# Optimization experiments

Hardware: AMD Instinct MI355X
Metric: run time of the kernel (lower is better)

Reference implementation:

```python
import jax, jax.numpy as jnp
import numpy as np


def setup_inputs() -> dict:
    key = jax.random.key(0)
    k1, k2 = jax.random.split(key)
    B, S_ENC, S_DEC, D = 8, 2048, 2048, 1024
    enc_outputs = jax.random.normal(k1, (B, S_ENC, D), dtype=jnp.float32)
    dec_outputs = jax.random.normal(k2, (B, S_DEC, D), dtype=jnp.float32)
    return {"enc_outputs": enc_outputs, "dec_outputs": dec_outputs}


def reference(enc_outputs, dec_outputs):
    # scores: [B, S_enc, S_dec] = enc @ dec^T (unscaled)
    a_t = jnp.einsum('bed,btd->bet', enc_outputs, dec_outputs)
    a_t = jax.nn.softmax(a_t, axis=-1)
    # context: [B, S_dec, D] = a_t^T @ enc
    c_t = jnp.einsum('bet,bed->btd', a_t, enc_outputs)
    return c_t
```

## Files before the change

### kernel.cpp

```cpp
#include <hip/hip_runtime.h>


typedef _Float16 half8 __attribute__((ext_vector_type(8)));
typedef _Float16 half4v __attribute__((ext_vector_type(4)));
typedef float floatx4 __attribute__((ext_vector_type(4)));

__device__ __forceinline__ void async_load16(const _Float16* g, void* l) {
  __builtin_amdgcn_global_load_lds(
      (const __attribute__((address_space(1))) void*)g,
      (__attribute__((address_space(3))) void*)l, 16, 0, 0);
}

template <typename OutT, bool NORM, bool STATS>
__global__ __launch_bounds__(512, 2) void gemm8p(
    const _Float16* __restrict__ A, const _Float16* __restrict__ Bt,
    OutT* __restrict__ C, const float* __restrict__ cstat,
    float2* __restrict__ part_out, int K, long strideA, long strideB,
    long strideC, int ldA, int ldB, int ldC) {
  extern __shared__ char smem_[];
  const int tid = threadIdx.x;
  const int lane = tid & 63;
  const int wave = tid >> 6;
  const int wm = wave >> 2;
  const int wn = wave & 3;
  const int l15 = lane & 15;
  const int lh = lane >> 4;

  const int gx = gridDim.x, gxy = gridDim.x * gridDim.y;
  int fid = blockIdx.z * gxy + blockIdx.y * gx + blockIdx.x;
  const int nwg = gxy * gridDim.z;
  fid = (fid & 7) * (nwg >> 3) + (fid >> 3);
  const int b = fid / gxy;
  const int rem = fid - b * gxy;
  const int m0 = (rem / gx) * 256;
  const int n0 = (rem % gx) * 256;

  A += (long)b * strideA + (long)m0 * ldA;
  Bt += (long)b * strideB + (long)n0 * ldB;
  C += (long)b * strideC;
  const float* cstatB = NORM ? cstat + (size_t)b * 2048 : nullptr;

  const int lb0 = l15 * 128 + ((lh ^ (l15 & 7)) << 4);
  const int lb1 = lb0 ^ 64;
  const char* aBuf[2] = {smem_ + wm * 16384, smem_ + 32768 + wm * 16384};
  const char* bBuf[2] = {
      smem_ + 65536 + (wn >> 1) * 16384 + (wn & 1) * 8192,
      smem_ + 98304 + (wn >> 1) * 16384 + (wn & 1) * 8192};
  char* aSlot[2] = {smem_, smem_ + 32768};
  char* bSlot[2] = {smem_ + 65536, smem_ + 98304};
  char* cLds = smem_ + 131072;

  const int srow = tid >> 3;
  const int skk = ((tid & 7) ^ (srow & 7)) << 3;
  const _Float16* Ast = A + (long)srow * ldA + skk;
  const _Float16* Bst = Bt + (long)srow * ldB + skk;
  const int dst = tid << 4;

  floatx4 acc[8][4] = {};
  half8 a[4][2], b0[2][2], b1[2][2];

  auto stage = [&](const _Float16* gs, int ld, int k0, char* slot) {
#pragma unroll
    for (int i = 0; i < 4; ++i)
      async_load16(gs + (long)(i * 64) * ld + k0, slot + i * 8192 + dst);
  };
  auto mm = [&](int mh, int nh, half8(&bb)[2][2]) {
    __builtin_amdgcn_s_setprio(1);
#pragma unroll
    for (int s = 0; s < 2; ++s)
#pragma unroll
      for (int q = 0; q < 4; ++q)
#pragma unroll
        for (int n = 0; n < 2; ++n)
          acc[mh * 4 + q][nh * 2 + n] = __builtin_amdgcn_mfma_f32_16x16x32_f16(
              a[q][s], bb[n][s], acc[mh * 4 + q][nh * 2 + n], 0, 0, 0);
    __builtin_amdgcn_s_setprio(0);
  };
  auto bar = [&]() { asm volatile("s_barrier" ::: "memory"); };

  auto quad4 = [&](int cur, int kst, int ebase, bool last) {
    const char* aB_ = aBuf[cur];
    const char* bB_ = bBuf[cur];
    if constexpr (NORM) {
      const int co = (ebase + skk) << 2;
      const float4 c0 = *(const float4*)(cLds + co);
      const float4 c1 = *(const float4*)(cLds + co + 16);
      const float cc[8] = {c0.x, c0.y, c0.z, c0.w, c1.x, c1.y, c1.z, c1.w};
#pragma unroll
      for (int i = 0; i < 4; ++i) {
        char* p = aSlot[cur] + i * 8192 + dst;
        half8 v = *(const half8*)p;
        half8 o;
#pragma unroll
        for (int j = 0; j < 8; ++j)
          o[j] = (_Float16)exp2f((float)v[j] * 1.44269504f + cc[j]);
        *(half8*)p = o;
      }
      asm volatile("s_waitcnt lgkmcnt(0)" ::: "memory");
      bar();
    }
#pragma unroll
    for (int q = 0; q < 4; ++q) {
      a[q][0] = *(const half8*)(aB_ + lb0 + q * 2048);
      a[q][1] = *(const half8*)(aB_ + lb1 + q * 2048);
    }
#pragma unroll
    for (int n = 0; n < 2; ++n) {
      b0[n][0] = *(const half8*)(bB_ + lb0 + n * 2048);
      b0[n][1] = *(const half8*)(bB_ + lb1 + n * 2048);
      b1[n][0] = *(const half8*)(bB_ + lb0 + (n + 2) * 2048);
      b1[n][1] = *(const half8*)(bB_ + lb1 + (n + 2) * 2048);
    }
    bar();
    mm(0, 0, b0);
    bar();
    bar();
    mm(0, 1, b1);
    bar();
#pragma unroll
    for (int q = 0; q < 4; ++q) {
      a[q][0] = *(const half8*)(aB_ + lb0 + (q + 4) * 2048);
      a[q][1] = *(const half8*)(aB_ + lb1 + (q + 4) * 2048);
    }
    if (kst >= 0) stage(Bst, ldB, kst, bSlot[cur]);
    bar();
    mm(1, 1, b1);
    bar();
    if (kst >= 0) stage(Ast, ldA, kst, aSlot[cur]);
    mm(1, 0, b0);
    if (last)
      asm volatile("s_waitcnt vmcnt(0)" ::: "memory");
    else
      asm volatile("s_waitcnt vmcnt(8)" ::: "memory");
    bar();
  };

  float4 cv;
  if constexpr (NORM) cv = *(const float4*)(cstatB + tid * 4);
  stage(Ast, ldA, 0, aSlot[0]);
  stage(Bst, ldB, 0, bSlot[0]);
  stage(Ast, ldA, 64, aSlot[1]);
  stage(Bst, ldB, 64, bSlot[1]);
  if constexpr (NORM) *(float4*)(cLds + (tid << 4)) = cv;
  asm volatile("s_waitcnt vmcnt(8) lgkmcnt(0)" ::: "memory");
  bar();

  const int NT = K >> 6;
  for (int i = 0; i < (NT >> 1) - 1; ++i) {
    quad4(0, (2 * i + 2) * 64, (2 * i) * 64, false);
    quad4(1, (2 * i + 3) * 64, (2 * i + 1) * 64, false);
  }
  quad4(0, -1, (NT - 2) * 64, true);
  quad4(1, -1, (NT - 1) * 64, true);

#pragma unroll
  for (int mf = 0; mf < 8; ++mf) {
    const long r0 = (long)(m0 + wm * 128 + mf * 16 + lh * 4);
#pragma unroll
    for (int nf = 0; nf < 4; ++nf) {
      const int cc = n0 + wn * 64 + nf * 16 + l15;
#pragma unroll
      for (int rr = 0; rr < 4; ++rr)
        C[(r0 + rr) * ldC + cc] = (OutT)acc[mf][nf][rr];
    }
  }

  if constexpr (STATS) {
    float2* sm = (float2*)smem_;
#pragma unroll
    for (int nf = 0; nf < 4; ++nf) {
      float x16[8][4];
#pragma unroll
      for (int mf = 0; mf < 8; ++mf)
#pragma unroll
        for (int rr = 0; rr < 4; ++rr)
          x16[mf][rr] = (float)(_Float16)acc[mf][nf][rr];
      float mx = -1e30f;
#pragma unroll
      for (int mf = 0; mf < 8; ++mf)
#pragma unroll
        for (int rr = 0; rr < 4; ++rr) mx = fmaxf(mx, x16[mf][rr]);
      float ss = 0.f;
#pragma unroll
      for (int mf = 0; mf < 8; ++mf)
#pragma unroll
        for (int rr = 0; rr < 4; ++rr) ss += __expf(x16[mf][rr] - mx);
#pragma unroll
      for (int d = 16; d <= 32; d <<= 1) {
        const float om = __shfl_xor(mx, d, 64);
        const float os = __shfl_xor(ss, d, 64);
        const float m2 = fmaxf(mx, om);
        ss = ss * __expf(mx - m2) + os * __expf(om - m2);
        mx = m2;
      }
      if (lh == 0) sm[wm * 256 + wn * 64 + nf * 16 + l15] = make_float2(mx, ss);
    }
    __syncthreads();
    if (tid < 256) {
      const float2 a0 = sm[tid], a1 = sm[256 + tid];
      const float m2 = fmaxf(a0.x, a1.x);
      const float s2 =
          a0.y * __expf(a0.x - m2) + a1.y * __expf(a1.x - m2);
      part_out[(size_t)(m0 >> 8) * 16384 + (size_t)b * 2048 + n0 + tid] =
          make_float2(m2, s2);
    }
  }
}

__global__ __launch_bounds__(256) void conv_enc(const float* __restrict__ E,
                                                _Float16* __restrict__ Eh,
                                                _Float16* __restrict__ EhT,
                                                int Se, int D) {
  __shared__ _Float16 T[64][72];
  const int b = blockIdx.z;
  const int d0 = blockIdx.x * 64;
  const int e0 = blockIdx.y * 64;
  const float* Eb = E + (size_t)b * Se * D;
  _Float16* Ehb = Eh + (size_t)b * Se * D;
  _Float16* EhTb = EhT + (size_t)b * D * Se;
  const int tid = threadIdx.x;
  const int tx = tid & 15;
  const int ty = tid >> 4;

  half4v h[4];
#pragma unroll
  for (int r = 0; r < 4; ++r) {
    const int e = e0 + ty * 4 + r;
    float4 v = *(const float4*)(Eb + (size_t)e * D + d0 + tx * 4);
    h[r][0] = (_Float16)v.x; h[r][1] = (_Float16)v.y;
    h[r][2] = (_Float16)v.z; h[r][3] = (_Float16)v.w;
    *(half4v*)(Ehb + (size_t)e * D + d0 + tx * 4) = h[r];
  }
#pragma unroll
  for (int c = 0; c < 4; ++c) {
    half4v w;
#pragma unroll
    for (int r = 0; r < 4; ++r) w[r] = h[r][c];
    *(half4v*)&T[tx * 4 + c][ty * 4] = w;
  }
  __syncthreads();
#pragma unroll
  for (int p = 0; p < 2; ++p) {
    const int idx = tid + p * 256;
    const int row = idx >> 3;
    const int ck = idx & 7;
    *(half8*)(EhTb + (size_t)(d0 + row) * Se + e0 + ck * 8) =
        *(const half8*)&T[row][ck * 8];
  }
}

__global__ __launch_bounds__(256) void conv_dec(const float* __restrict__ X,
                                                _Float16* __restrict__ Y) {
  const size_t i = ((size_t)blockIdx.x * 256 + threadIdx.x) * 8;
  float4 a = *(const float4*)(X + i);
  float4 b = *(const float4*)(X + i + 4);
  half8 h;
  h[0] = (_Float16)a.x; h[1] = (_Float16)a.y;
  h[2] = (_Float16)a.z; h[3] = (_Float16)a.w;
  h[4] = (_Float16)b.x; h[5] = (_Float16)b.y;
  h[6] = (_Float16)b.z; h[7] = (_Float16)b.w;
  *(half8*)(Y + i) = h;
}

__global__ __launch_bounds__(256) void stats_combine(
    const float2* __restrict__ part, float* __restrict__ cstat) {
  const int idx = blockIdx.x * 256 + threadIdx.x;
  float2 a = part[idx];
#pragma unroll
  for (int tc = 1; tc < 8; ++tc) {
    const float2 o = part[tc * 16384 + idx];
    const float m2 = fmaxf(a.x, o.x);
    a.y = a.y * __expf(a.x - m2) + o.y * __expf(o.x - m2);
    a.x = m2;
  }
  cstat[idx] = -(a.x * 1.44269504f + log2f(a.y));
}

extern "C" void kernel_launch(void* const* d_in, const int* in_sizes, int n_in,
                              void* d_out, int out_size, void* d_ws,
                              size_t ws_size, hipStream_t stream) {
  const float* enc = (const float*)d_in[0];
  const float* dec = (const float*)d_in[1];
  float* out = (float*)d_out;

  const int B = 8, SE = 2048, SD = 2048, D = 1024;
  char* ws = (char*)d_ws;
  _Float16* enc_h = (_Float16*)ws;
  _Float16* dec_h = (_Float16*)(ws + 33554432);
  _Float16* enc_hT = (_Float16*)(ws + 67108864);
  _Float16* ST = (_Float16*)(ws + 100663296);
  float* cstat = (float*)(ws + 167772160);
  float2* part2 = (float2*)(ws + 167903232);

  static int smem_set = 0;
  if (!smem_set) {
    (void)hipFuncSetAttribute(
        reinterpret_cast<const void*>(&gemm8p<_Float16, false, true>),
        hipFuncAttributeMaxDynamicSharedMemorySize, 131072);
    (void)hipFuncSetAttribute(
        reinterpret_cast<const void*>(&gemm8p<float, true, false>),
        hipFuncAttributeMaxDynamicSharedMemorySize, 139264);
    smem_set = 1;
  }

  conv_enc<<<dim3(D / 64, SE / 64, B), 256, 0, stream>>>(enc, enc_h, enc_hT,
                                                         SE, D);
  conv_dec<<<dim3((size_t)B * SD * D / 2048), 256, 0, stream>>>(dec, dec_h);
  gemm8p<_Float16, false, true>
      <<<dim3(SE / 256, SD / 256, B), 512, 131072, stream>>>(
          dec_h, enc_h, ST, nullptr, part2, D, (long)SD * D, (long)SE * D,
          (long)SD * SE, D, D, SE);
  stats_combine<<<dim3(64), 256, 0, stream>>>(part2, cstat);
  gemm8p<float, true, false>
      <<<dim3(D / 256, SD / 256, B), 512, 139264, stream>>>(
          ST, enc_hT, out, cstat, nullptr, SE, (long)SD * SE, (long)D * SE,
          (long)SD * D, SE, SE, D);
}
```

Baseline: 351.6 us.

## Unfuse softmax exponentiation from the second GEMM into a streaming kernel

Removes the in-loop exp2 normalization of the A tiles, and its extra LDS read-modify-write and barrier, from the context GEMM. Adds a separate elementwise kernel that applies exp2(s*log2e + cstat) to the score matrix once and writes normalized probabilities P into workspace previously holding the fp16 enc/dec copies. The second GEMM becomes a plain GEMM with no per-tile exp work, which was previously repeated for every output column block, and its LDS request drops. The cost is an extra full read and write of the 64 MB score matrix through HBM and one more kernel launch.

Measured after the change: 321.0 us. 1.1x faster.

```diff
diff --git a/kernel.cpp b/kernel.cpp
--- a/kernel.cpp
+++ b/kernel.cpp
@@ -11,12 +11,11 @@
       (__attribute__((address_space(3))) void*)l, 16, 0, 0);
 }
 
-template <typename OutT, bool NORM, bool STATS>
+template <typename OutT, bool STATS>
 __global__ __launch_bounds__(512, 2) void gemm8p(
     const _Float16* __restrict__ A, const _Float16* __restrict__ Bt,
-    OutT* __restrict__ C, const float* __restrict__ cstat,
-    float2* __restrict__ part_out, int K, long strideA, long strideB,
-    long strideC, int ldA, int ldB, int ldC) {
+    OutT* __restrict__ C, float2* __restrict__ part_out, int K, long strideA,
+    long strideB, long strideC, int ldA, int ldB, int ldC) {
   extern __shared__ char smem_[];
   const int tid = threadIdx.x;
   const int lane = tid & 63;
@@ -38,7 +37,6 @@
   A += (long)b * strideA + (long)m0 * ldA;
   Bt += (long)b * strideB + (long)n0 * ldB;
   C += (long)b * strideC;
-  const float* cstatB = NORM ? cstat + (size_t)b * 2048 : nullptr;
 
   const int lb0 = l15 * 128 + ((lh ^ (l15 & 7)) << 4);
   const int lb1 = lb0 ^ 64;
@@ -48,7 +46,6 @@
       smem_ + 98304 + (wn >> 1) * 16384 + (wn & 1) * 8192};
   char* aSlot[2] = {smem_, smem_ + 32768};
   char* bSlot[2] = {smem_ + 65536, smem_ + 98304};
-  char* cLds = smem_ + 131072;
 
   const int srow = tid >> 3;
   const int skk = ((tid & 7) ^ (srow & 7)) << 3;
@@ -78,27 +75,9 @@
   };
   auto bar = [&]() { asm volatile("s_barrier" ::: "memory"); };
 
-  auto quad4 = [&](int cur, int kst, int ebase, bool last) {
+  auto quad4 = [&](int cur, int kst, bool last) {
     const char* aB_ = aBuf[cur];
     const char* bB_ = bBuf[cur];
-    if constexpr (NORM) {
-      const int co = (ebase + skk) << 2;
-      const float4 c0 = *(const float4*)(cLds + co);
-      const float4 c1 = *(const float4*)(cLds + co + 16);
-      const float cc[8] = {c0.x, c0.y, c0.z, c0.w, c1.x, c1.y, c1.z, c1.w};
-#pragma unroll
-      for (int i = 0; i < 4; ++i) {
-        char* p = aSlot[cur] + i * 8192 + dst;
-        half8 v = *(const half8*)p;
-        half8 o;
-#pragma unroll
-        for (int j = 0; j < 8; ++j)
-          o[j] = (_Float16)exp2f((float)v[j] * 1.44269504f + cc[j]);
-        *(half8*)p = o;
-      }
-      asm volatile("s_waitcnt lgkmcnt(0)" ::: "memory");
-      bar();
-    }
 #pragma unroll
     for (int q = 0; q < 4; ++q) {
       a[q][0] = *(const half8*)(aB_ + lb0 + q * 2048);
@@ -135,23 +114,20 @@
     bar();
   };
 
-  float4 cv;
-  if constexpr (NORM) cv = *(const float4*)(cstatB + tid * 4);
   stage(Ast, ldA, 0, aSlot[0]);
   stage(Bst, ldB, 0, bSlot[0]);
   stage(Ast, ldA, 64, aSlot[1]);
   stage(Bst, ldB, 64, bSlot[1]);
-  if constexpr (NORM) *(float4*)(cLds + (tid << 4)) = cv;
-  asm volatile("s_waitcnt vmcnt(8) lgkmcnt(0)" ::: "memory");
+  asm volatile("s_waitcnt vmcnt(8)" ::: "memory");
   bar();
 
   const int NT = K >> 6;
   for (int i = 0; i < (NT >> 1) - 1; ++i) {
-    quad4(0, (2 * i + 2) * 64, (2 * i) * 64, false);
-    quad4(1, (2 * i + 3) * 64, (2 * i + 1) * 64, false);
-  }
-  quad4(0, -1, (NT - 2) * 64, true);
-  quad4(1, -1, (NT - 1) * 64, true);
+    quad4(0, (2 * i + 2) * 64, false);
+    quad4(1, (2 * i + 3) * 64, false);
+  }
+  quad4(0, -1, true);
+  quad4(1, -1, true);
 
 #pragma unroll
   for (int mf = 0; mf < 8; ++mf) {
@@ -276,6 +252,27 @@
   cstat[idx] = -(a.x * 1.44269504f + log2f(a.y));
 }
 
+__global__ __launch_bounds__(256) void norm_stream(
+    const _Float16* __restrict__ ST, const float* __restrict__ cstat,
+    _Float16* __restrict__ P) {
+  const int b = blockIdx.y;
+  const int t0 = blockIdx.x * 4;
+  const int e = threadIdx.x * 8;
+  float c_[8];
+  *(float4*)c_ = *(const float4*)(cstat + (size_t)b * 2048 + e);
+  *(float4*)(c_ + 4) = *(const float4*)(cstat + (size_t)b * 2048 + e + 4);
+  const size_t base = ((size_t)b * 2048 + t0) * 2048 + e;
+#pragma unroll
+  for (int r = 0; r < 4; ++r) {
+    half8 v = *(const half8*)(ST + base + (size_t)r * 2048);
+    half8 o;
+#pragma unroll
+    for (int j = 0; j < 8; ++j)
+      o[j] = (_Float16)exp2f((float)v[j] * 1.44269504f + c_[j]);
+    *(half8*)(P + base + (size_t)r * 2048) = o;
+  }
+}
+
 extern "C" void kernel_launch(void* const* d_in, const int* in_sizes, int n_in,
                               void* d_out, int out_size, void* d_ws,
                               size_t ws_size, hipStream_t stream) {
@@ -287,6 +284,7 @@
   char* ws = (char*)d_ws;
   _Float16* enc_h = (_Float16*)ws;
   _Float16* dec_h = (_Float16*)(ws + 33554432);
+  _Float16* P = (_Float16*)ws;
   _Float16* enc_hT = (_Float16*)(ws + 67108864);
   _Float16* ST = (_Float16*)(ws + 100663296);
   float* cstat = (float*)(ws + 167772160);
@@ -295,24 +293,23 @@
   static int smem_set = 0;
   if (!smem_set) {
     (void)hipFuncSetAttribute(
-        reinterpret_cast<const void*>(&gemm8p<_Float16, false, true>),
+        reinterpret_cast<const void*>(&gemm8p<_Float16, true>),
         hipFuncAttributeMaxDynamicSharedMemorySize, 131072);
     (void)hipFuncSetAttribute(
-        reinterpret_cast<const void*>(&gemm8p<float, true, false>),
-        hipFuncAttributeMaxDynamicSharedMemorySize, 139264);
+        reinterpret_cast<const void*>(&gemm8p<float, false>),
+        hipFuncAttributeMaxDynamicSharedMemorySize, 131072);
     smem_set = 1;
   }
 
   conv_enc<<<dim3(D / 64, SE / 64, B), 256, 0, stream>>>(enc, enc_h, enc_hT,
                                                          SE, D);
   conv_dec<<<dim3((size_t)B * SD * D / 2048), 256, 0, stream>>>(dec, dec_h);
-  gemm8p<_Float16, false, true>
-      <<<dim3(SE / 256, SD / 256, B), 512, 131072, stream>>>(
-          dec_h, enc_h, ST, nullptr, part2, D, (long)SD * D, (long)SE * D,
-          (long)SD * SE, D, D, SE);
+  gemm8p<_Float16, true><<<dim3(SE / 256, SD / 256, B), 512, 131072, stream>>>(
+      dec_h, enc_h, ST, part2, D, (long)SD * D, (long)SE * D, (long)SD * SE,
+      D, D, SE);
   stats_combine<<<dim3(64), 256, 0, stream>>>(part2, cstat);
-  gemm8p<float, true, false>
-      <<<dim3(D / 256, SD / 256, B), 512, 139264, stream>>>(
-          ST, enc_hT, out, cstat, nullptr, SE, (long)SD * SE, (long)D * SE,
-          (long)SD * D, SE, SE, D);
-}
+  norm_stream<<<dim3(512, B), 256, 0, stream>>>(ST, cstat, P);
+  gemm8p<float, false><<<dim3(D / 256, SD / 256, B), 512, 131072, stream>>>(
+      P, enc_hT, out, nullptr, SE, (long)SD * SE, (long)D * SE, (long)SD * D,
+      SE, SE, D);
+}
```
